# Optimization experiments

Hardware: AMD Instinct MI355X
Metric: run time of the kernel (lower is better)

The kernel has to match this reference:

```python
import jax, jax.numpy as jnp
import numpy as np

TEMPERATURE = 0.07
TOP_MARGIN = 0.95
BOTTOM_MARGIN = 0.05

BATCH = 8192
DIM = 1024


def setup_inputs() -> dict:
    key = jax.random.key(0)
    kA, kB = jax.random.split(key)
    embedding_A = jax.random.normal(kA, (BATCH, DIM), dtype=jnp.float32)
    embedding_B = jax.random.normal(kB, (BATCH, DIM), dtype=jnp.float32)
    return {"embedding_A": embedding_A, "embedding_B": embedding_B}


def _l2norm(x):
    return x * jax.lax.rsqrt(jnp.sum(x * x, axis=-1, keepdims=True))


def reference(embedding_A, embedding_B):
    a = _l2norm(embedding_A)
    b = _l2norm(embedding_B)
    B = a.shape[0]
    sim = a @ b.T                                   # [B, B]
    pos = jnp.diagonal(sim)                         # [B]
    eye = jnp.eye(B, dtype=bool)
    upper = pos[:, None] * TOP_MARGIN
    lower = pos[:, None] * BOTTOM_MARGIN
    neg_mask = (sim <= upper) & (sim >= lower) & ~eye   # [B, B]

    # Per-row CE over [positive, hard negatives] == masked logsumexp - pos/tau.
    z = sim / TEMPERATURE
    full_mask = neg_mask | eye                      # positive always included
    masked = jnp.where(full_mask, z, -jnp.inf)
    m = jnp.max(masked, axis=1, keepdims=True)      # finite: diag always present
    lse = m[:, 0] + jnp.log(jnp.sum(jnp.exp(masked - m), axis=1))
    per_row = lse - pos / TEMPERATURE               # [B]

    valid = jnp.any(neg_mask, axis=1)               # rows with >=1 negative
    count = jnp.sum(valid)
    total = jnp.sum(jnp.where(valid, per_row, 0.0))
    return total / jnp.maximum(count, 1).astype(total.dtype)
```

## Files before the change

### kernel.cpp

```cpp
#include <hip/hip_runtime.h>
#include <hip/hip_bf16.h>

#define BATCH 8192
#define DIM   1024
#define INV_TAU (1.0f / 0.07f)
#define TOPM 0.95f
#define BOTM 0.05f

#define BM 256
#define BN 256
#define BK 64
#define NT (DIM / BK)

typedef __attribute__((ext_vector_type(4))) float f32x4;
typedef __attribute__((ext_vector_type(8))) short bf16x8;

typedef __attribute__((address_space(3))) void       lds_void_t;
typedef const __attribute__((address_space(1))) void gbl_void_t;

__device__ inline void async_copy16(const void* g, void* l) {
    __builtin_amdgcn_global_load_lds((gbl_void_t*)g, (lds_void_t*)l, 16, 0, 0);
}

__device__ inline unsigned short f2bf(float f) {
    __hip_bfloat16 h = __float2bfloat16(f);
    return *reinterpret_cast<unsigned short*>(&h);
}

__global__ __launch_bounds__(256) void prep_kernel(
    const float* __restrict__ A, const float* __restrict__ B,
    unsigned short* __restrict__ An, unsigned short* __restrict__ Bn,
    float* __restrict__ pos, float* __restrict__ S)
{
    int row = blockIdx.x;
    int t = threadIdx.x;
    const float4* a4 = (const float4*)(A + (size_t)row * DIM);
    const float4* b4 = (const float4*)(B + (size_t)row * DIM);
    float4 av = a4[t];
    float4 bv = b4[t];
    float sa = av.x*av.x + av.y*av.y + av.z*av.z + av.w*av.w;
    float sb = bv.x*bv.x + bv.y*bv.y + bv.z*bv.z + bv.w*bv.w;
    float dp = av.x*bv.x + av.y*bv.y + av.z*bv.z + av.w*bv.w;
    #pragma unroll
    for (int d = 32; d > 0; d >>= 1) {
        sa += __shfl_down(sa, d);
        sb += __shfl_down(sb, d);
        dp += __shfl_down(dp, d);
    }
    __shared__ float red[3][4];
    int lane = t & 63, w = t >> 6;
    if (lane == 0) { red[0][w] = sa; red[1][w] = sb; red[2][w] = dp; }
    __syncthreads();
    sa = red[0][0] + red[0][1] + red[0][2] + red[0][3];
    sb = red[1][0] + red[1][1] + red[1][2] + red[1][3];
    dp = red[2][0] + red[2][1] + red[2][2] + red[2][3];
    float ra = rsqrtf(sa);
    float rb = rsqrtf(sb);
    if (t == 0) {
        pos[row] = dp * ra * rb;
        S[row] = 0.0f;
    }
    ushort4 oa, ob;
    oa.x = f2bf(av.x * ra); oa.y = f2bf(av.y * ra);
    oa.z = f2bf(av.z * ra); oa.w = f2bf(av.w * ra);
    ob.x = f2bf(bv.x * rb); ob.y = f2bf(bv.y * rb);
    ob.z = f2bf(bv.z * rb); ob.w = f2bf(bv.w * rb);
    ((ushort4*)(An + (size_t)row * DIM))[t] = oa;
    ((ushort4*)(Bn + (size_t)row * DIM))[t] = ob;
}

__global__ __launch_bounds__(512, 1) void sim_loss_kernel(
    const unsigned short* __restrict__ An, const unsigned short* __restrict__ Bn,
    const float* __restrict__ pos, float* __restrict__ S)
{
    __shared__ char lds[131072];

    int tid  = threadIdx.x;
    int lane = tid & 63;
    int wave = tid >> 6;
    int wm = wave >> 2, wn = wave & 3;
    int fr = lane & 15;
    int q  = lane >> 4;

    int bid = blockIdx.x;

#define BASES(g, rB, cB) do {                                                        \
    int xcd_ = bid & 7, jj_ = bid >> 3;                                              \
    int qr_ = (g) >> 1, qc_ = ((g) & 1) ^ (qr_ & 1);                                 \
    (rB) = (qr_ * 16 + (xcd_ >> 1) * 4 + (jj_ >> 3)) * BM;                           \
    (cB) = (qc_ * 16 + (xcd_ & 1) * 8 + (jj_ & 7)) * BN;                             \
} while (0)

    f32x4 acc[8][4] = {};
    bf16x8 a[4][2];
    bf16x8 b0[2][2];
    bf16x8 b1[2][2];

    int sw = (fr & 7) << 4;
    int c0 = (q * 16) ^ sw;
    int c1 = (64 + q * 16) ^ sw;
    int aRow = (wm * 128 + fr) * 128;
    int bRow = (wn * 64 + fr) * 128;

    int strow = tid >> 3;
    int scb   = ((tid & 7) * 16) ^ ((strow & 7) << 4);
    int ldst = tid * 16;

#define PANELS(rB, cB, pA, pB) do {                                                  \
    (pA) = (const char*)An + (size_t)((rB) + strow) * 2048 + scb;                    \
    (pB) = (const char*)Bn + (size_t)((cB) + strow) * 2048 + scb;                    \
} while (0)

#define STAGE(gbase, u, h, ldsdst) do {                                              \
    async_copy16((gbase) + (size_t)(h) * 262144 + (size_t)(u) * 128,                 \
                 (ldsdst) + (h) * 16384 + ldst);                                     \
    async_copy16((gbase) + (size_t)(h) * 262144 + 131072 + (size_t)(u) * 128,        \
                 (ldsdst) + (h) * 16384 + 8192 + ldst);                              \
} while (0)

#define LDA_(p, mh) do {                                                             \
    const char* _s = lds + (p) * 32768;                                              \
    _Pragma("unroll") for (int m = 0; m < 4; ++m) {                                  \
        a[m][0] = *(const bf16x8*)(_s + aRow + (mh) * 8192 + m * 2048 + c0);         \
        a[m][1] = *(const bf16x8*)(_s + aRow + (mh) * 8192 + m * 2048 + c1);         \
    }                                                                                \
} while (0)

#define LDB_(arr, p, nh) do {                                                        \
    const char* _s = lds + 65536 + (p) * 32768;                                      \
    _Pragma("unroll") for (int n = 0; n < 2; ++n) {                                  \
        arr[n][0] = *(const bf16x8*)(_s + bRow + (nh) * 4096 + n * 2048 + c0);       \
        arr[n][1] = *(const bf16x8*)(_s + bRow + (nh) * 4096 + n * 2048 + c1);       \
    }                                                                                \
} while (0)

#define MM_(barr, mo, no) do {                                                       \
    _Pragma("unroll") for (int m = 0; m < 4; ++m)                                    \
    _Pragma("unroll") for (int n = 0; n < 2; ++n) {                                  \
        acc[(mo)+m][(no)+n] = __builtin_amdgcn_mfma_f32_16x16x32_bf16(               \
            a[m][0], barr[n][0], acc[(mo)+m][(no)+n], 0, 0, 0);                      \
        acc[(mo)+m][(no)+n] = __builtin_amdgcn_mfma_f32_16x16x32_bf16(               \
            a[m][1], barr[n][1], acc[(mo)+m][(no)+n], 0, 0, 0);                      \
    }                                                                                \
} while (0)

#define BAR() __builtin_amdgcn_s_barrier()
#define SCH() __builtin_amdgcn_sched_barrier(0)
#define LGKM0() asm volatile("s_waitcnt lgkmcnt(0)" ::: "memory")
#define VMC(n)  asm volatile("s_waitcnt vmcnt(" #n ")" ::: "memory")
#define PRI1() __builtin_amdgcn_s_setprio(1)
#define PRI0() __builtin_amdgcn_s_setprio(0)

#define KTILE(p, pA_, uA, pB_, uB) do {                                              \
    char* stA = lds + ((p) ^ 1) * 32768;                                             \
    char* stB = lds + 65536 + (p) * 32768;                                           \
                                                 \
    BAR(); SCH();                                                                    \
    LDA_((p), 0); LDB_(b0, (p), 0); LDB_(b1, (p), 1);                                \
    STAGE((pA_), (uA), 0, stA); STAGE((pA_), (uA), 1, stA);                          \
    PRI1(); MM_(b0, 0, 0); MM_(b1, 0, 2); PRI0();                                    \
    LGKM0();                                                                         \
                                                 \
    BAR(); SCH();                                                                    \
    LDA_((p), 1);                                                                    \
    STAGE((pB_), (uB), 0, stB); STAGE((pB_), (uB), 1, stB);                          \
    PRI1(); MM_(b1, 4, 2); MM_(b0, 4, 0); PRI0();                                    \
    LGKM0(); VMC(4);                                                                 \
} while (0)

    int rowB, colB;
    BASES(0, rowB, colB);
    const char *gAc, *gBc;
    PANELS(rowB, colB, gAc, gBc);

    STAGE(gAc, 0, 0, lds);
    STAGE(gAc, 0, 1, lds);
    STAGE(gBc, 0, 0, lds + 65536);
    STAGE(gBc, 0, 1, lds + 65536);
    STAGE(gBc, 1, 0, lds + 98304);
    STAGE(gBc, 1, 1, lds + 98304);
    VMC(4);

    #pragma unroll 1
    for (int g = 0; g < 4; ++g) {
        int gn = (g < 3) ? g + 1 : 3;
        int rowBn, colBn;
        BASES(gn, rowBn, colBn);
        const char *gAn2, *gBn2;
        PANELS(rowBn, colBn, gAn2, gBn2);

        #pragma unroll 1
        for (int tt = 0; tt < 7; ++tt) {
            KTILE(0, gAc, 2 * tt + 1, gBc, 2 * tt + 2);
            KTILE(1, gAc, 2 * tt + 2, gBc, 2 * tt + 3);
        }
        KTILE(0, gAc, 15, gBn2, 0);
        KTILE(1, gAn2, 0, gBn2, 1);

        #pragma unroll
        for (int m = 0; m < 8; ++m) {
            #pragma unroll
            for (int j2 = 0; j2 < 4; ++j2) {
                int i = rowB + wm * 128 + m * 16 + q * 4 + j2;
                float p  = pos[i];
                float up = TOPM * p, lo = BOTM * p;
                float rs = 0.0f;
                #pragma unroll
                for (int n = 0; n < 4; ++n) {
                    float sv = acc[m][n][j2];
                    int col = colB + wn * 64 + n * 16 + fr;
                    if (sv <= up && sv >= lo && col != i)
                        rs += __expf((sv - p) * INV_TAU);
                }
                #pragma unroll
                for (int d = 1; d < 16; d <<= 1)
                    rs += __shfl_xor(rs, d);
                if (fr == 0 && rs != 0.0f)
                    atomicAdd(&S[i], rs);
            }
        }
        #pragma unroll
        for (int m2 = 0; m2 < 8; ++m2)
            #pragma unroll
            for (int n2 = 0; n2 < 4; ++n2)
                acc[m2][n2] = (f32x4){0.0f, 0.0f, 0.0f, 0.0f};

        gAc = gAn2; gBc = gBn2; rowB = rowBn; colB = colBn;
    }
    LGKM0();
    VMC(0);

#undef BASES
#undef PANELS
#undef STAGE
#undef LDA_
#undef LDB_
#undef MM_
#undef BAR
#undef SCH
#undef LGKM0
#undef VMC
#undef PRI1
#undef PRI0
#undef KTILE
}

__global__ __launch_bounds__(256) void finalize_kernel(
    const float* __restrict__ S, float* __restrict__ out)
{
    int t = threadIdx.x;
    float tot = 0.0f;
    int c = 0;
    for (int i = t; i < BATCH; i += 256) {
        float s = S[i];
        if (s > 0.0f) { tot += log1pf(s); c += 1; }
    }
    #pragma unroll
    for (int d = 32; d > 0; d >>= 1) {
        tot += __shfl_down(tot, d);
        c   += __shfl_down(c, d);
    }
    __shared__ float st[4];
    __shared__ int   sc[4];
    int lane = t & 63, w = t >> 6;
    if (lane == 0) { st[w] = tot; sc[w] = c; }
    __syncthreads();
    if (t == 0) {
        float T = st[0] + st[1] + st[2] + st[3];
        int   C = sc[0] + sc[1] + sc[2] + sc[3];
        out[0] = T / (float)(C > 0 ? C : 1);
    }
}

extern "C" void kernel_launch(void* const* d_in, const int* in_sizes, int n_in,
                              void* d_out, int out_size, void* d_ws, size_t ws_size,
                              hipStream_t stream) {
    const float* A = (const float*)d_in[0];
    const float* B = (const float*)d_in[1];

    char* ws = (char*)d_ws;
    unsigned short* An = (unsigned short*)ws;
    unsigned short* Bn = An + (size_t)BATCH * DIM;
    float* pos = (float*)(Bn + (size_t)BATCH * DIM);
    float* S   = pos + BATCH;
    float* out = (float*)d_out;

    prep_kernel<<<BATCH, 256, 0, stream>>>(A, B, An, Bn, pos, S);
    sim_loss_kernel<<<256, 512, 0, stream>>>(An, Bn, pos, S);
    finalize_kernel<<<1, 256, 0, stream>>>(S, out);
}
```

Before: 216.6 us.

## Switch similarity GEMM to FP8 with 32x32x64 scaled MFMA and LDS row reduction

Normalized embeddings are now quantized to FP8 instead of BF16 in the prep kernel. The GEMM uses the MI355X scaled 32x32x64 f8f6f4 MFMA with K=128 per tile, which halves global and LDS traffic and doubles peak matrix throughput. Per-row partial sums are now combined in LDS before a single global atomic per row. The cost is FP8 precision on the similarities, which feed hard threshold comparisons, so the loss value may move noticeably away from the reference.

```diff
diff --git a/kernel.cpp b/kernel.cpp
--- a/kernel.cpp
+++ b/kernel.cpp
@@ -9,11 +9,11 @@
 
 #define BM 256
 #define BN 256
-#define BK 64
+#define BK 128
 #define NT (DIM / BK)
 
-typedef __attribute__((ext_vector_type(4))) float f32x4;
-typedef __attribute__((ext_vector_type(8))) short bf16x8;
+typedef __attribute__((ext_vector_type(8)))  int   v8i;
+typedef __attribute__((ext_vector_type(16))) float f32x16;
 
 typedef __attribute__((address_space(3))) void       lds_void_t;
 typedef const __attribute__((address_space(1))) void gbl_void_t;
@@ -22,14 +22,9 @@
     __builtin_amdgcn_global_load_lds((gbl_void_t*)g, (lds_void_t*)l, 16, 0, 0);
 }
 
-__device__ inline unsigned short f2bf(float f) {
-    __hip_bfloat16 h = __float2bfloat16(f);
-    return *reinterpret_cast<unsigned short*>(&h);
-}
-
 __global__ __launch_bounds__(256) void prep_kernel(
     const float* __restrict__ A, const float* __restrict__ B,
-    unsigned short* __restrict__ An, unsigned short* __restrict__ Bn,
+    unsigned char* __restrict__ An, unsigned char* __restrict__ Bn,
     float* __restrict__ pos, float* __restrict__ S)
 {
     int row = blockIdx.x;
@@ -60,27 +55,28 @@
         pos[row] = dp * ra * rb;
         S[row] = 0.0f;
     }
-    ushort4 oa, ob;
-    oa.x = f2bf(av.x * ra); oa.y = f2bf(av.y * ra);
-    oa.z = f2bf(av.z * ra); oa.w = f2bf(av.w * ra);
-    ob.x = f2bf(bv.x * rb); ob.y = f2bf(bv.y * rb);
-    ob.z = f2bf(bv.z * rb); ob.w = f2bf(bv.w * rb);
-    ((ushort4*)(An + (size_t)row * DIM))[t] = oa;
-    ((ushort4*)(Bn + (size_t)row * DIM))[t] = ob;
+    int ua = 0, ub = 0;
+    ua = __builtin_amdgcn_cvt_pk_fp8_f32(av.x * ra, av.y * ra, ua, false);
+    ua = __builtin_amdgcn_cvt_pk_fp8_f32(av.z * ra, av.w * ra, ua, true);
+    ub = __builtin_amdgcn_cvt_pk_fp8_f32(bv.x * rb, bv.y * rb, ub, false);
+    ub = __builtin_amdgcn_cvt_pk_fp8_f32(bv.z * rb, bv.w * rb, ub, true);
+    ((int*)(An + (size_t)row * DIM))[t] = ua;
+    ((int*)(Bn + (size_t)row * DIM))[t] = ub;
 }
 
 __global__ __launch_bounds__(512, 1) void sim_loss_kernel(
-    const unsigned short* __restrict__ An, const unsigned short* __restrict__ Bn,
+    const unsigned char* __restrict__ An, const unsigned char* __restrict__ Bn,
     const float* __restrict__ pos, float* __restrict__ S)
 {
-    __shared__ char lds[131072];
+    __shared__ char lds[132096];
+    float* rowAcc = (float*)(lds + 131072);
 
     int tid  = threadIdx.x;
     int lane = tid & 63;
     int wave = tid >> 6;
     int wm = wave >> 2, wn = wave & 3;
-    int fr = lane & 15;
-    int q  = lane >> 4;
+    int l31 = lane & 31;
+    int hi  = lane >> 5;
 
     int bid = blockIdx.x;
 
@@ -91,57 +87,63 @@
     (cB) = (qc_ * 16 + (xcd_ & 1) * 8 + (jj_ & 7)) * BN;                             \
 } while (0)
 
-    f32x4 acc[8][4] = {};
-    bf16x8 a[4][2];
-    bf16x8 b0[2][2];
-    bf16x8 b1[2][2];
-
-    int sw = (fr & 7) << 4;
-    int c0 = (q * 16) ^ sw;
-    int c1 = (64 + q * 16) ^ sw;
-    int aRow = (wm * 128 + fr) * 128;
-    int bRow = (wn * 64 + fr) * 128;
+    f32x16 acc[4][2] = {};
+    v8i aF[4];
+    v8i bF[2][2];
+
+    int sw = (lane & 7) << 4;
+    int cc00 = (hi * 32) ^ sw;
+    int cc01 = (hi * 32 + 16) ^ sw;
+    int cc10 = (64 + hi * 32) ^ sw;
+    int cc11 = (64 + hi * 32 + 16) ^ sw;
+    int aRow = (wm * 128 + l31) * 128;
+    int bRow = (wn * 64 + l31) * 128;
 
     int strow = tid >> 3;
     int scb   = ((tid & 7) * 16) ^ ((strow & 7) << 4);
     int ldst = tid * 16;
 
 #define PANELS(rB, cB, pA, pB) do {                                                  \
-    (pA) = (const char*)An + (size_t)((rB) + strow) * 2048 + scb;                    \
-    (pB) = (const char*)Bn + (size_t)((cB) + strow) * 2048 + scb;                    \
+    (pA) = (const char*)An + (size_t)((rB) + strow) * 1024 + scb;                    \
+    (pB) = (const char*)Bn + (size_t)((cB) + strow) * 1024 + scb;                    \
 } while (0)
 
 #define STAGE(gbase, u, h, ldsdst) do {                                              \
-    async_copy16((gbase) + (size_t)(h) * 262144 + (size_t)(u) * 128,                 \
+    async_copy16((gbase) + (size_t)(h) * 131072 + (size_t)(u) * 128,                 \
                  (ldsdst) + (h) * 16384 + ldst);                                     \
-    async_copy16((gbase) + (size_t)(h) * 262144 + 131072 + (size_t)(u) * 128,        \
+    async_copy16((gbase) + (size_t)(h) * 131072 + 65536 + (size_t)(u) * 128,         \
                  (ldsdst) + (h) * 16384 + 8192 + ldst);                              \
 } while (0)
 
-#define LDA_(p, mh) do {                                                             \
+#define PACK8(d0, d1) (v8i){d0.x, d0.y, d0.z, d0.w, d1.x, d1.y, d1.z, d1.w}
+
+#define LDA_(p, c_a, c_b) do {                                                       \
     const char* _s = lds + (p) * 32768;                                              \
-    _Pragma("unroll") for (int m = 0; m < 4; ++m) {                                  \
-        a[m][0] = *(const bf16x8*)(_s + aRow + (mh) * 8192 + m * 2048 + c0);         \
-        a[m][1] = *(const bf16x8*)(_s + aRow + (mh) * 8192 + m * 2048 + c1);         \
+    _Pragma("unroll") for (int mt = 0; mt < 4; ++mt) {                               \
+        int4 d0 = *(const int4*)(_s + aRow + mt * 4096 + (c_a));                     \
+        int4 d1 = *(const int4*)(_s + aRow + mt * 4096 + (c_b));                     \
+        aF[mt] = PACK8(d0, d1);                                                      \
     }                                                                                \
 } while (0)
 
-#define LDB_(arr, p, nh) do {                                                        \
+#define LDBB_(p) do {                                                                \
     const char* _s = lds + 65536 + (p) * 32768;                                      \
-    _Pragma("unroll") for (int n = 0; n < 2; ++n) {                                  \
-        arr[n][0] = *(const bf16x8*)(_s + bRow + (nh) * 4096 + n * 2048 + c0);       \
-        arr[n][1] = *(const bf16x8*)(_s + bRow + (nh) * 4096 + n * 2048 + c1);       \
+    _Pragma("unroll") for (int nt = 0; nt < 2; ++nt) {                               \
+        int4 e0 = *(const int4*)(_s + bRow + nt * 4096 + cc00);                      \
+        int4 e1 = *(const int4*)(_s + bRow + nt * 4096 + cc01);                      \
+        bF[nt][0] = PACK8(e0, e1);                                                   \
+        int4 e2 = *(const int4*)(_s + bRow + nt * 4096 + cc10);                      \
+        int4 e3 = *(const int4*)(_s + bRow + nt * 4096 + cc11);                      \
+        bF[nt][1] = PACK8(e2, e3);                                                   \
     }                                                                                \
 } while (0)
 
-#define MM_(barr, mo, no) do {                                                       \
-    _Pragma("unroll") for (int m = 0; m < 4; ++m)                                    \
-    _Pragma("unroll") for (int n = 0; n < 2; ++n) {                                  \
-        acc[(mo)+m][(no)+n] = __builtin_amdgcn_mfma_f32_16x16x32_bf16(               \
-            a[m][0], barr[n][0], acc[(mo)+m][(no)+n], 0, 0, 0);                      \
-        acc[(mo)+m][(no)+n] = __builtin_amdgcn_mfma_f32_16x16x32_bf16(               \
-            a[m][1], barr[n][1], acc[(mo)+m][(no)+n], 0, 0, 0);                      \
-    }                                                                                \
+#define MMK_(ks) do {                                                                \
+    _Pragma("unroll") for (int mt = 0; mt < 4; ++mt)                                 \
+    _Pragma("unroll") for (int nt = 0; nt < 2; ++nt)                                 \
+        acc[mt][nt] = __builtin_amdgcn_mfma_scale_f32_32x32x64_f8f6f4(               \
+            aF[mt], bF[nt][ks], acc[mt][nt], 0, 0,                                   \
+            0, 0x7F7F7F7F, 0, 0x7F7F7F7F);                                           \
 } while (0)
 
 #define BAR() __builtin_amdgcn_s_barrier()
@@ -154,17 +156,17 @@
 #define KTILE(p, pA_, uA, pB_, uB) do {                                              \
     char* stA = lds + ((p) ^ 1) * 32768;                                             \
     char* stB = lds + 65536 + (p) * 32768;                                           \
-                                                 \
+                                                                  \
     BAR(); SCH();                                                                    \
-    LDA_((p), 0); LDB_(b0, (p), 0); LDB_(b1, (p), 1);                                \
+    LDA_((p), cc00, cc01); LDBB_((p));                                               \
     STAGE((pA_), (uA), 0, stA); STAGE((pA_), (uA), 1, stA);                          \
-    PRI1(); MM_(b0, 0, 0); MM_(b1, 0, 2); PRI0();                                    \
+    PRI1(); MMK_(0); PRI0();                                                         \
     LGKM0();                                                                         \
-                                                 \
+                                                                  \
     BAR(); SCH();                                                                    \
-    LDA_((p), 1);                                                                    \
+    LDA_((p), cc10, cc11);                                                           \
     STAGE((pB_), (uB), 0, stB); STAGE((pB_), (uB), 1, stB);                          \
-    PRI1(); MM_(b1, 4, 2); MM_(b0, 4, 0); PRI0();                                    \
+    PRI1(); MMK_(1); PRI0();                                                         \
     LGKM0(); VMC(4);                                                                 \
 } while (0)
 
@@ -190,40 +192,50 @@
         PANELS(rowBn, colBn, gAn2, gBn2);
 
         #pragma unroll 1
-        for (int tt = 0; tt < 7; ++tt) {
+        for (int tt = 0; tt < 3; ++tt) {
             KTILE(0, gAc, 2 * tt + 1, gBc, 2 * tt + 2);
             KTILE(1, gAc, 2 * tt + 2, gBc, 2 * tt + 3);
         }
-        KTILE(0, gAc, 15, gBn2, 0);
+        KTILE(0, gAc, 7, gBn2, 0);
         KTILE(1, gAn2, 0, gBn2, 1);
 
+        BAR();
+        if (tid < 256) rowAcc[tid] = 0.0f;
+        BAR();
         #pragma unroll
-        for (int m = 0; m < 8; ++m) {
+        for (int mt = 0; mt < 4; ++mt) {
             #pragma unroll
-            for (int j2 = 0; j2 < 4; ++j2) {
-                int i = rowB + wm * 128 + m * 16 + q * 4 + j2;
+            for (int r = 0; r < 16; ++r) {
+                int io = wm * 128 + mt * 32 + (r & 3) + 8 * (r >> 2) + 4 * hi;
+                int i  = rowB + io;
                 float p  = pos[i];
                 float up = TOPM * p, lo = BOTM * p;
                 float rs = 0.0f;
                 #pragma unroll
-                for (int n = 0; n < 4; ++n) {
-                    float sv = acc[m][n][j2];
-                    int col = colB + wn * 64 + n * 16 + fr;
+                for (int nt = 0; nt < 2; ++nt) {
+                    float sv = acc[mt][nt][r];
+                    int col = colB + wn * 64 + nt * 32 + l31;
                     if (sv <= up && sv >= lo && col != i)
                         rs += __expf((sv - p) * INV_TAU);
                 }
                 #pragma unroll
-                for (int d = 1; d < 16; d <<= 1)
+                for (int d = 1; d < 32; d <<= 1)
                     rs += __shfl_xor(rs, d);
-                if (fr == 0 && rs != 0.0f)
-                    atomicAdd(&S[i], rs);
+                if (l31 == 0 && rs != 0.0f)
+                    atomicAdd(&rowAcc[io], rs);
             }
         }
+        LGKM0();
+        BAR();
+        if (tid < 256) {
+            float v = rowAcc[tid];
+            if (v > 0.0f) atomicAdd(&S[rowB + tid], v);
+        }
         #pragma unroll
-        for (int m2 = 0; m2 < 8; ++m2)
+        for (int m2 = 0; m2 < 4; ++m2)
             #pragma unroll
-            for (int n2 = 0; n2 < 4; ++n2)
-                acc[m2][n2] = (f32x4){0.0f, 0.0f, 0.0f, 0.0f};
+            for (int n2 = 0; n2 < 2; ++n2)
+                acc[m2][n2] = (f32x16)(0.0f);
 
         gAc = gAn2; gBc = gBn2; rowB = rowBn; colB = colBn;
     }
@@ -233,9 +245,10 @@
 #undef BASES
 #undef PANELS
 #undef STAGE
+#undef PACK8
 #undef LDA_
-#undef LDB_
-#undef MM_
+#undef LDBB_
+#undef MMK_
 #undef BAR
 #undef SCH
 #undef LGKM0
@@ -279,8 +292,8 @@
     const float* B = (const float*)d_in[1];
 
     char* ws = (char*)d_ws;
-    unsigned short* An = (unsigned short*)ws;
-    unsigned short* Bn = An + (size_t)BATCH * DIM;
+    unsigned char* An = (unsigned char*)ws;
+    unsigned char* Bn = An + (size_t)BATCH * DIM;
     float* pos = (float*)(Bn + (size_t)BATCH * DIM);
     float* S   = pos + BATCH;
     float* out = (float*)d_out;
```

Result: slower. 337.7 us (+55.9%).

## Restructure K-tile pipeline into four barrier-separated MFMA phases with finer staging

Applied to the files above, without the earlier changes.

Splits each K-tile step of the GEMM main loop into four phases. Each phase issues a half-tile global-to-LDS stage, waits on partial lgkmcnt/vmcnt counts, and runs one MFMA block between barriers, where before there were two larger phases. The A/B LDS double-buffer assignment and the prologue staging order change to match. The aim is to spread global loads and LDS reads more evenly across MFMA work and improve latency hiding, at the cost of more barriers per tile and tight wait counts that must stay correct.

```diff
diff --git a/kernel.cpp b/kernel.cpp
--- a/kernel.cpp
+++ b/kernel.cpp
@@ -146,26 +146,31 @@
 
 #define BAR() __builtin_amdgcn_s_barrier()
 #define SCH() __builtin_amdgcn_sched_barrier(0)
-#define LGKM0() asm volatile("s_waitcnt lgkmcnt(0)" ::: "memory")
+#define LGKM(n) asm volatile("s_waitcnt lgkmcnt(" #n ")" ::: "memory")
 #define VMC(n)  asm volatile("s_waitcnt vmcnt(" #n ")" ::: "memory")
 #define PRI1() __builtin_amdgcn_s_setprio(1)
 #define PRI0() __builtin_amdgcn_s_setprio(0)
 
-#define KTILE(p, pA_, uA, pB_, uB) do {                                              \
-    char* stA = lds + ((p) ^ 1) * 32768;                                             \
-    char* stB = lds + 65536 + (p) * 32768;                                           \
-                                                 \
+#define KTILE(p, gA1, uA1, gB1, uB1, gA2, uA2) do {                                  \
+    char* stA1 = lds + ((p) ^ 1) * 32768;                                            \
+    char* stB1 = lds + 65536 + ((p) ^ 1) * 32768;                                    \
+    char* stA2 = lds + (p) * 32768;                                                  \
+                                                             \
+    LDA_((p), 0); LDB_(b0, (p), 0); STAGE((gA1), (uA1), 1, stA1);                    \
+    LGKM(8); BAR(); SCH();                                                           \
+    LGKM(0); PRI1(); MM_(b0, 0, 0); PRI0(); BAR(); SCH();                            \
+                                                             \
+    LDB_(b1, (p), 1); STAGE((gB1), (uB1), 0, stB1);                                  \
     BAR(); SCH();                                                                    \
-    LDA_((p), 0); LDB_(b0, (p), 0); LDB_(b1, (p), 1);                                \
-    STAGE((pA_), (uA), 0, stA); STAGE((pA_), (uA), 1, stA);                          \
-    PRI1(); MM_(b0, 0, 0); MM_(b1, 0, 2); PRI0();                                    \
-    LGKM0();                                                                         \
-                                                 \
+    LGKM(0); PRI1(); MM_(b1, 0, 2); PRI0(); BAR(); SCH();                            \
+                                                             \
+    LDA_((p), 1); STAGE((gB1), (uB1), 1, stB1);                                      \
     BAR(); SCH();                                                                    \
-    LDA_((p), 1);                                                                    \
-    STAGE((pB_), (uB), 0, stB); STAGE((pB_), (uB), 1, stB);                          \
-    PRI1(); MM_(b1, 4, 2); MM_(b0, 4, 0); PRI0();                                    \
-    LGKM0(); VMC(4);                                                                 \
+    LGKM(0); PRI1(); MM_(b1, 4, 2); PRI0(); BAR(); SCH();                            \
+                                                             \
+    STAGE((gA2), (uA2), 0, stA2);                                                    \
+    BAR(); SCH();                                                                    \
+    PRI1(); MM_(b0, 4, 0); PRI0(); VMC(2); BAR(); SCH();                             \
 } while (0)
 
     int rowB, colB;
@@ -177,9 +182,10 @@
     STAGE(gAc, 0, 1, lds);
     STAGE(gBc, 0, 0, lds + 65536);
     STAGE(gBc, 0, 1, lds + 65536);
-    STAGE(gBc, 1, 0, lds + 98304);
-    STAGE(gBc, 1, 1, lds + 98304);
-    VMC(4);
+    STAGE(gAc, 1, 0, lds + 32768);
+    VMC(2);
+    BAR();
+    SCH();
 
     #pragma unroll 1
     for (int g = 0; g < 4; ++g) {
@@ -191,11 +197,12 @@
 
         #pragma unroll 1
         for (int tt = 0; tt < 7; ++tt) {
-            KTILE(0, gAc, 2 * tt + 1, gBc, 2 * tt + 2);
-            KTILE(1, gAc, 2 * tt + 2, gBc, 2 * tt + 3);
+            int t0 = 2 * tt;
+            KTILE(0, gAc, t0 + 1, gBc, t0 + 1, gAc, t0 + 2);
+            KTILE(1, gAc, t0 + 2, gBc, t0 + 2, gAc, t0 + 3);
         }
-        KTILE(0, gAc, 15, gBn2, 0);
-        KTILE(1, gAn2, 0, gBn2, 1);
+        KTILE(0, gAc, 15, gBc, 15, gAn2, 0);
+        KTILE(1, gAn2, 0, gBn2, 0, gAn2, 1);
 
         #pragma unroll
         for (int m = 0; m < 8; ++m) {
@@ -227,7 +234,7 @@
 
         gAc = gAn2; gBc = gBn2; rowB = rowBn; colB = colBn;
     }
-    LGKM0();
+    LGKM(0);
     VMC(0);
 
 #undef BASES
@@ -238,7 +245,7 @@
 #undef MM_
 #undef BAR
 #undef SCH
-#undef LGKM0
+#undef LGKM
 #undef VMC
 #undef PRI1
 #undef PRI0
```

New measurement: 222.1 us. +2.6%, slower.
